# Performance work log

Hardware: AMD Instinct MI355X
Metric: run time of the kernel (lower is better)

Reference implementation:

```python
import jax, jax.numpy as jnp
import numpy as np
from math import erf, pi, sqrt, exp

D = 2048
TARGET_BITS = 2.5
N_HIGH = 1024  # round(D * frac)
N_LOW = D - N_HIGH
HIGH_MSE_BITS = 2  # ceil(2.5) - 1
LOW_MSE_BITS = 1   # floor(2.5) - 1


def _phi(x):
    return np.exp(-0.5 * x * x) / np.sqrt(2.0 * np.pi)


def _Phi(x):
    return 0.5 * (1.0 + np.vectorize(erf)(x / np.sqrt(2.0)))


def lloyd_max_centroids(bits: int) -> np.ndarray:
    """Lloyd-Max optimal scalar quantizer centroids for N(0,1), 2**bits levels."""
    L = 2 ** bits
    c = np.linspace(-2.0, 2.0, L)
    for _ in range(200):
        b = 0.5 * (c[:-1] + c[1:])                      # decision boundaries
        edges = np.concatenate([[-1e9], b, [1e9]])
        lo, hi = edges[:-1], edges[1:]
        mass = _Phi(hi) - _Phi(lo)
        c = (_phi(lo) - _phi(hi)) / np.maximum(mass, 1e-12)  # conditional mean
    return c.astype(np.float32)


def generate_rotation_matrix(d: int, seed: int) -> np.ndarray:
    rng = np.random.default_rng(seed)
    A = rng.standard_normal((d, d)).astype(np.float64)
    Q, R = np.linalg.qr(A)
    Q = Q * np.sign(np.diag(R))[None, :]
    return Q.astype(np.float32)


def setup_inputs() -> dict:
    key = jax.random.key(0)
    kq, kk = jax.random.split(key)
    queries = jax.random.normal(kq, (1024, D), dtype=jnp.float32)
    keys = jax.random.normal(kk, (4096, D), dtype=jnp.float32)
    Pi = jnp.asarray(generate_rotation_matrix(D, seed=42 + 2000))
    high_centroids = jnp.asarray(lloyd_max_centroids(HIGH_MSE_BITS))  # (4,)
    low_centroids = jnp.asarray(lloyd_max_centroids(LOW_MSE_BITS))    # (2,)
    rng = np.random.default_rng(42)
    S_high = jnp.asarray(rng.standard_normal((N_HIGH, N_HIGH)).astype(np.float32))
    rng2 = np.random.default_rng(42 + 1000)
    S_low = jnp.asarray(rng2.standard_normal((N_LOW, N_LOW)).astype(np.float32))
    return {"queries": queries, "keys": keys, "Pi": Pi,
            "high_centroids": high_centroids, "low_centroids": low_centroids,
            "S_high": S_high, "S_low": S_low}


def _quantize_group(y, centroids, S):
    # nearest-centroid scalar quantization per channel
    idx = jnp.argmin(jnp.abs(y[..., None] - centroids), axis=-1)  # (bk, n_ch)
    y_mse = centroids[idx]
    residual = y - y_mse
    residual_norm = jnp.linalg.norm(residual, axis=-1)            # (bk,)
    signs = jnp.sign(residual @ S.T)                              # (bk, m)
    return y_mse, signs, residual_norm


def _ip_group(q_ch, y_mse, signs, residual_norm, S):
    m = S.shape[0]
    term1 = q_ch @ y_mse.T                                        # (bq, bk)
    # QJL estimator: <q, r> ~ sqrt(pi/2)/m * ||r|| * <S q, sign(S r)>
    term2 = (jnp.sqrt(jnp.float32(pi / 2)) / m) * ((q_ch @ S.T) @ signs.T) * residual_norm[None, :]
    return term1 + term2


def reference(queries, keys, Pi, high_centroids, low_centroids, S_high, S_low):
    # ---- quantize keys ----
    vec_norm = jnp.linalg.norm(keys, axis=-1)                     # (bk,)
    k_n = keys / (vec_norm[:, None] + 1e-8)
    y = k_n @ Pi.T
    yh, yl = y[:, :N_HIGH], y[:, N_HIGH:]
    kmse_h, sg_h, rn_h = _quantize_group(yh, high_centroids, S_high)
    kmse_l, sg_l, rn_l = _quantize_group(yl, low_centroids, S_low)
    # ---- inner product estimate ----
    q_rot = queries @ Pi.T
    qh, ql = q_rot[:, :N_HIGH], q_rot[:, N_HIGH:]
    ip = _ip_group(qh, kmse_h, sg_h, rn_h, S_high) + _ip_group(ql, kmse_l, sg_l, rn_l, S_low)
    return ip * vec_norm[None, :]                                 # (bq, bk)
```

## Files before the change

### kernel.cpp

```cpp
#include <hip/hip_runtime.h>
#include <math.h>

#ifndef M_PI
#define M_PI 3.14159265358979323846
#endif

typedef __attribute__((ext_vector_type(8))) __bf16 bf16x8;
typedef __attribute__((ext_vector_type(4))) float f32x4;
typedef __attribute__((ext_vector_type(8))) unsigned short ushort8;

__device__ __forceinline__ unsigned short f2bf(float x) {
    unsigned int u = __float_as_uint(x);
    unsigned int r = (u + 0x7FFFu + ((u >> 16) & 1u)) >> 16;
    return (unsigned short)r;
}

__global__ __launch_bounds__(256)
void norm_np_k(const float* __restrict__ keys,
               float* __restrict__ den,
               float* __restrict__ vnorm)
{
#pragma clang fp contract(off)
    const int tid = threadIdx.x;
    const int row_l = tid >> 4;
    const int blk = tid & 15;
    const int row = blockIdx.x * 16 + row_l;
    const float* a = keys + (size_t)row * 2048 + blk * 128;

    float r0 = a[0]*a[0], r1 = a[1]*a[1], r2 = a[2]*a[2], r3 = a[3]*a[3];
    float r4 = a[4]*a[4], r5 = a[5]*a[5], r6 = a[6]*a[6], r7 = a[7]*a[7];
    for (int i = 8; i < 128; i += 8) {
        r0 += a[i+0]*a[i+0]; r1 += a[i+1]*a[i+1];
        r2 += a[i+2]*a[i+2]; r3 += a[i+3]*a[i+3];
        r4 += a[i+4]*a[i+4]; r5 += a[i+5]*a[i+5];
        r6 += a[i+6]*a[i+6]; r7 += a[i+7]*a[i+7];
    }
    float bsum = ((r0 + r1) + (r2 + r3)) + ((r4 + r5) + (r6 + r7));

    __shared__ float bs[16][16];
    bs[row_l][blk] = bsum;
    __syncthreads();
    if (blk == 0) {
        const float* b = bs[row_l];
        float q0 = ((b[0] + b[1]) + (b[2] + b[3])) + ((b[4] + b[5]) + (b[6] + b[7]));
        float q1 = ((b[8] + b[9]) + (b[10] + b[11])) + ((b[12] + b[13]) + (b[14] + b[15]));
        float s = q0 + q1;
        float n = (float)sqrt((double)s);
        den[row] = n + 1e-8f;
        vnorm[row] = n;
    }
}

__global__ __launch_bounds__(256)
void f2bf_k(const float* __restrict__ in, unsigned short* __restrict__ out)
{
    const int i = (blockIdx.x * 256 + threadIdx.x) * 8;
    float4 v0 = *(const float4*)(in + i);
    float4 v1 = *(const float4*)(in + i + 4);
    ushort8 o;
    o[0] = f2bf(v0.x); o[1] = f2bf(v0.y); o[2] = f2bf(v0.z); o[3] = f2bf(v0.w);
    o[4] = f2bf(v1.x); o[5] = f2bf(v1.y); o[6] = f2bf(v1.z); o[7] = f2bf(v1.w);
    *(ushort8*)(out + i) = o;
}

template <int EPI, int DIVA>
__global__ __launch_bounds__(256)
void gemm_dec_k(const float* __restrict__ A, int lda,
                const float* __restrict__ B, int ldb,
                float* __restrict__ Cf, unsigned short* __restrict__ Cb,
                int ldc, int K,
                const float* __restrict__ dena,
                const float* __restrict__ rv)
{
#pragma clang fp contract(off)
    __shared__ float As[16][132];
    __shared__ float Bs[16][132];

    const int tid = threadIdx.x;
    const int tr = tid >> 4;
    const int tc = tid & 15;
    const int row0 = blockIdx.y * 128;
    const int col0 = blockIdx.x * 128;
    const int sr = tid >> 1;
    const int sk = (tid & 1) * 8;

    const float dv = DIVA ? dena[row0 + sr] : 1.0f;
    const float* ga = A + (size_t)(row0 + sr) * lda + sk;
    const float* gb = B + (size_t)(col0 + sr) * ldb + sk;

    float acc[8][8] = {};

    for (int k0 = 0; k0 < K; k0 += 16) {
        float av[8], bv[8];
        *(float4*)(av)     = *(const float4*)(ga + k0);
        *(float4*)(av + 4) = *(const float4*)(ga + k0 + 4);
        *(float4*)(bv)     = *(const float4*)(gb + k0);
        *(float4*)(bv + 4) = *(const float4*)(gb + k0 + 4);
        if (DIVA) {
            #pragma unroll
            for (int u = 0; u < 8; ++u) av[u] = av[u] / dv;
        }
        __syncthreads();
        #pragma unroll
        for (int u = 0; u < 8; ++u) {
            As[sk + u][sr] = av[u];
            Bs[sk + u][sr] = bv[u];
        }
        __syncthreads();
        #pragma unroll
        for (int kk = 0; kk < 16; ++kk) {
            float a[8], b[8];
            *(float4*)(a)     = *(const float4*)&As[kk][tr * 8];
            *(float4*)(a + 4) = *(const float4*)&As[kk][tr * 8 + 4];
            *(float4*)(b)     = *(const float4*)&Bs[kk][tc * 8];
            *(float4*)(b + 4) = *(const float4*)&Bs[kk][tc * 8 + 4];
            #pragma unroll
            for (int i = 0; i < 8; ++i)
                #pragma unroll
                for (int j = 0; j < 8; ++j)
                    acc[i][j] = fmaf(a[i], b[j], acc[i][j]);
        }
    }

    if (EPI == 0) {
        #pragma unroll
        for (int i = 0; i < 8; ++i) {
            const int r = row0 + tr * 8 + i;
            #pragma unroll
            for (int j = 0; j < 8; ++j)
                Cf[(size_t)r * ldc + col0 + tc * 8 + j] = acc[i][j];
        }
    } else {
        #pragma unroll
        for (int i = 0; i < 8; ++i) {
            const int r = row0 + tr * 8 + i;
            const float s = rv[r];
            #pragma unroll
            for (int j = 0; j < 8; ++j) {
                const float t = acc[i][j];
                const float v = (t > 0.0f) ? s : ((t < 0.0f) ? -s : 0.0f);
                Cb[(size_t)r * ldc + col0 + tc * 8 + j] = f2bf(v);
            }
        }
    }
}

__global__ __launch_bounds__(256)
void quant_k(float* __restrict__ Y,
             unsigned short* __restrict__ Bmse,
             const float* __restrict__ ch,
             const float* __restrict__ cl,
             float* __restrict__ sc_h,
             float* __restrict__ sc_l,
             double coefd)
{
#pragma clang fp contract(off)
    const int row = blockIdx.x;
    const int tid = threadIdx.x;
    const int c0 = tid * 8;
    const float h0 = ch[0], h1 = ch[1], h2 = ch[2], h3 = ch[3];
    const float l0 = cl[0], l1 = cl[1];

    float y[8], res[8];
    ushort8 cb;
    *(float4*)(y)     = *(const float4*)(Y + (size_t)row * 2048 + c0);
    *(float4*)(y + 4) = *(const float4*)(Y + (size_t)row * 2048 + c0 + 4);

    const bool high = (tid < 128);
    float ss = 0.0f;
    #pragma unroll
    for (int j = 0; j < 8; ++j) {
        const float v = y[j];
        float cbest;
        if (high) {
            cbest = h0;
            float bd = fabsf(v - h0), dd;
            dd = fabsf(v - h1); if (dd < bd) { bd = dd; cbest = h1; }
            dd = fabsf(v - h2); if (dd < bd) { bd = dd; cbest = h2; }
            dd = fabsf(v - h3); if (dd < bd) { bd = dd; cbest = h3; }
        } else {
            cbest = (fabsf(v - l1) < fabsf(v - l0)) ? l1 : l0;
        }
        res[j] = v - cbest;
        cb[j] = f2bf(cbest);
        ss += res[j] * res[j];
    }
    *(float4*)(Y + (size_t)row * 2048 + c0)     = *(float4*)(res);
    *(float4*)(Y + (size_t)row * 2048 + c0 + 4) = *(float4*)(res + 4);
    *(ushort8*)(Bmse + (size_t)row * 4096 + c0) = cb;

    __shared__ float sm[256];
    sm[tid] = ss;
    __syncthreads();
    for (int o = 64; o > 0; o >>= 1) {
        if ((tid & 127) < o) sm[tid] += sm[tid + o];
        __syncthreads();
    }
    if (tid == 0)   sc_h[row] = (float)(coefd * sqrt((double)sm[0]));
    if (tid == 128) sc_l[row] = (float)(coefd * sqrt((double)sm[128]));
}

template <int EPI>
__global__ __launch_bounds__(256)
void gemm_mfma_k(const unsigned short* __restrict__ A, int lda,
                 const unsigned short* __restrict__ B, int ldb,
                 float* __restrict__ Cf, unsigned short* __restrict__ Cb,
                 int ldc, int K, const float* __restrict__ colscale)
{
    __shared__ unsigned short As[128][40];
    __shared__ unsigned short Bs[128][40];

    const int tid = threadIdx.x;
    const int lane = tid & 63;
    const int wid = tid >> 6;
    const int wm = wid >> 1;
    const int wn = wid & 1;
    const int row0 = blockIdx.y * 128;
    const int col0 = blockIdx.x * 128;
    const int sr = tid >> 1;
    const int sk = (tid & 1) * 16;
    const int frow = lane & 15;
    const int fk = (lane >> 4) * 8;

    const unsigned short* ga = A + (size_t)(row0 + sr) * lda + sk;
    const unsigned short* gb = B + (size_t)(col0 + sr) * ldb + sk;

    f32x4 acc[4][4] = {};

    for (int k0 = 0; k0 < K; k0 += 32) {
        ushort8 a0 = *(const ushort8*)(ga + k0);
        ushort8 a1 = *(const ushort8*)(ga + k0 + 8);
        ushort8 b0 = *(const ushort8*)(gb + k0);
        ushort8 b1 = *(const ushort8*)(gb + k0 + 8);
        __syncthreads();
        *(ushort8*)&As[sr][sk]     = a0;
        *(ushort8*)&As[sr][sk + 8] = a1;
        *(ushort8*)&Bs[sr][sk]     = b0;
        *(ushort8*)&Bs[sr][sk + 8] = b1;
        __syncthreads();

        bf16x8 af[4], bfr[4];
        #pragma unroll
        for (int mi = 0; mi < 4; ++mi)
            af[mi] = *(const bf16x8*)&As[wm * 64 + mi * 16 + frow][fk];
        #pragma unroll
        for (int ni = 0; ni < 4; ++ni)
            bfr[ni] = *(const bf16x8*)&Bs[wn * 64 + ni * 16 + frow][fk];
        #pragma unroll
        for (int mi = 0; mi < 4; ++mi)
            #pragma unroll
            for (int ni = 0; ni < 4; ++ni)
                acc[mi][ni] = __builtin_amdgcn_mfma_f32_16x16x32_bf16(
                    af[mi], bfr[ni], acc[mi][ni], 0, 0, 0);
    }

    const int drow = (lane >> 4) * 4;
    const int dcol = lane & 15;
    #pragma unroll
    for (int mi = 0; mi < 4; ++mi) {
        #pragma unroll
        for (int ni = 0; ni < 4; ++ni) {
            const int c = col0 + wn * 64 + ni * 16 + dcol;
            const float cs = (EPI == 1) ? colscale[c] : 0.0f;
            #pragma unroll
            for (int rg = 0; rg < 4; ++rg) {
                const int r = row0 + wm * 64 + mi * 16 + drow + rg;
                const float v = acc[mi][ni][rg];
                if (EPI == 1) Cf[(size_t)r * ldc + c] = v * cs;
                else          Cb[(size_t)r * ldc + c] = f2bf(v);
            }
        }
    }
}

extern "C" void kernel_launch(void* const* d_in, const int* in_sizes, int n_in,
                              void* d_out, int out_size, void* d_ws, size_t ws_size,
                              hipStream_t stream)
{
    const float* queries = (const float*)d_in[0];
    const float* keys    = (const float*)d_in[1];
    const float* Pi      = (const float*)d_in[2];
    const float* ch      = (const float*)d_in[3];
    const float* cl      = (const float*)d_in[4];
    const float* S_high  = (const float*)d_in[5];
    const float* S_low   = (const float*)d_in[6];
    float* out = (float*)d_out;

    char* ws = (char*)d_ws;
    float*          Y     = (float*)(ws);
    unsigned short* Bbig  = (unsigned short*)(ws + ((size_t)32 << 20));
    unsigned short* Abig  = (unsigned short*)(ws + ((size_t)64 << 20));
    unsigned short* Qb    = (unsigned short*)(ws + ((size_t)72 << 20));
    unsigned short* Pib   = (unsigned short*)(ws + ((size_t)76 << 20));
    unsigned short* Sbh   = (unsigned short*)(ws + ((size_t)84 << 20));
    unsigned short* Sbl   = (unsigned short*)(ws + ((size_t)86 << 20));
    float*          den   = (float*)(ws + ((size_t)88 << 20));
    float*          vnorm = (float*)(ws + ((size_t)88 << 20) + 16384);
    float*          sc_h  = (float*)(ws + ((size_t)88 << 20) + 32768);
    float*          sc_l  = (float*)(ws + ((size_t)88 << 20) + 49152);

    const double coefd = sqrt(M_PI / 2.0) / 1024.0;

    norm_np_k<<<256, 256, 0, stream>>>(keys, den, vnorm);

    f2bf_k<<<1024, 256, 0, stream>>>(queries, Qb);
    f2bf_k<<<2048, 256, 0, stream>>>(Pi, Pib);
    f2bf_k<<<512, 256, 0, stream>>>(S_high, Sbh);
    f2bf_k<<<512, 256, 0, stream>>>(S_low, Sbl);

    gemm_dec_k<0, 1><<<dim3(16, 32), 256, 0, stream>>>(
        keys, 2048, Pi, 2048, Y, nullptr, 2048, 2048, den, nullptr);

    quant_k<<<4096, 256, 0, stream>>>(Y, Bbig, ch, cl, sc_h, sc_l, coefd);

    gemm_dec_k<1, 0><<<dim3(8, 32), 256, 0, stream>>>(
        Y, 2048, S_high, 1024, nullptr, Bbig + 2048, 4096, 1024, nullptr, sc_h);
    gemm_dec_k<1, 0><<<dim3(8, 32), 256, 0, stream>>>(
        Y + 1024, 2048, S_low, 1024, nullptr, Bbig + 3072, 4096, 1024, nullptr, sc_l);

    gemm_mfma_k<2><<<dim3(16, 8), 256, 0, stream>>>(
        Qb, 2048, Pib, 2048, nullptr, Abig, 4096, 2048, nullptr);
    gemm_mfma_k<2><<<dim3(8, 8), 256, 0, stream>>>(
        Abig, 4096, Sbh, 1024, nullptr, Abig + 2048, 4096, 1024, nullptr);
    gemm_mfma_k<2><<<dim3(8, 8), 256, 0, stream>>>(
        Abig + 1024, 4096, Sbl, 1024, nullptr, Abig + 3072, 4096, 1024, nullptr);

    gemm_mfma_k<1><<<dim3(32, 8), 256, 0, stream>>>(
        Abig, 4096, Bbig, 4096, out, nullptr, 4096, 4096, vnorm);
}
```

Before: 940.9 us.

## Prefetch and double-buffer fp32 GEMM fragments, batch per-group GEMMs via grid z

The fp32 exact GEMM now prefetches the next global K-slab into registers while it computes the current one. It also double-buffers the LDS fragment reads and remaps each thread's 8x8 tile into two 4-wide strips spaced 64 apart, so LDS reads avoid bank conflicts and stores can be vectorized. The key normalization divide moves into a separate elementwise kernel that writes a normalized copy of the keys. The high and low QJL sign GEMMs, and the two S-projection MFMA GEMMs, each merge into a single launch using blockIdx.z. This removes launches and fills more CUs, at the cost of an extra 32MB read/write pass for the normalized keys.

New measurement: 829.2 us. -11.9%, faster.

```diff
diff --git a/kernel.cpp b/kernel.cpp
--- a/kernel.cpp
+++ b/kernel.cpp
@@ -8,6 +8,7 @@
 typedef __attribute__((ext_vector_type(8))) __bf16 bf16x8;
 typedef __attribute__((ext_vector_type(4))) float f32x4;
 typedef __attribute__((ext_vector_type(8))) unsigned short ushort8;
+typedef __attribute__((ext_vector_type(4))) unsigned short ushort4v;
 
 __device__ __forceinline__ unsigned short f2bf(float x) {
     unsigned int u = __float_as_uint(x);
@@ -52,6 +53,23 @@
 }
 
 __global__ __launch_bounds__(256)
+void kn_k(const float* __restrict__ keys,
+          const float* __restrict__ den,
+          float* __restrict__ kn)
+{
+#pragma clang fp contract(off)
+    const int idx = (blockIdx.x * 256 + threadIdx.x) * 8;
+    const int row = idx >> 11;
+    const float d = den[row];
+    float4 v0 = *(const float4*)(keys + idx);
+    float4 v1 = *(const float4*)(keys + idx + 4);
+    v0.x /= d; v0.y /= d; v0.z /= d; v0.w /= d;
+    v1.x /= d; v1.y /= d; v1.z /= d; v1.w /= d;
+    *(float4*)(kn + idx) = v0;
+    *(float4*)(kn + idx + 4) = v1;
+}
+
+__global__ __launch_bounds__(256)
 void f2bf_k(const float* __restrict__ in, unsigned short* __restrict__ out)
 {
     const int i = (blockIdx.x * 256 + threadIdx.x) * 8;
@@ -63,86 +81,116 @@
     *(ushort8*)(out + i) = o;
 }
 
-template <int EPI, int DIVA>
-__global__ __launch_bounds__(256)
-void gemm_dec_k(const float* __restrict__ A, int lda,
-                const float* __restrict__ B, int ldb,
+template <int EPI>
+__global__ __launch_bounds__(256)
+void gemm_dec_k(const float* __restrict__ A, int lda, int a_zoff,
+                const float* __restrict__ B0, const float* __restrict__ B1,
+                int ldb,
                 float* __restrict__ Cf, unsigned short* __restrict__ Cb,
-                int ldc, int K,
-                const float* __restrict__ dena,
-                const float* __restrict__ rv)
+                int c_zoff, int ldc, int K,
+                const float* __restrict__ rv0, const float* __restrict__ rv1)
 {
 #pragma clang fp contract(off)
     __shared__ float As[16][132];
     __shared__ float Bs[16][132];
 
+    const int z = blockIdx.z;
+    const float* Ap = A + (size_t)z * a_zoff;
+    const float* Bp = z ? B1 : B0;
+    const float* rvp = z ? rv1 : rv0;
+    unsigned short* Cbp = (EPI == 1) ? (Cb + (size_t)z * c_zoff) : nullptr;
+
     const int tid = threadIdx.x;
-    const int tr = tid >> 4;
-    const int tc = tid & 15;
+    const int tr4 = (tid >> 4) * 4;
+    const int tc4 = (tid & 15) * 4;
     const int row0 = blockIdx.y * 128;
     const int col0 = blockIdx.x * 128;
     const int sr = tid >> 1;
     const int sk = (tid & 1) * 8;
 
-    const float dv = DIVA ? dena[row0 + sr] : 1.0f;
-    const float* ga = A + (size_t)(row0 + sr) * lda + sk;
-    const float* gb = B + (size_t)(col0 + sr) * ldb + sk;
-
-    float acc[8][8] = {};
+    const float* ga = Ap + (size_t)(row0 + sr) * lda + sk;
+    const float* gb = Bp + (size_t)(col0 + sr) * ldb + sk;
+
+    float acc[2][2][4][4] = {};
+    float sa[8], sb[8];
+
+#define LOADSTAGE(off) do { \
+    *(float4*)(sa)     = *(const float4*)(ga + (off)); \
+    *(float4*)(sa + 4) = *(const float4*)(ga + (off) + 4); \
+    *(float4*)(sb)     = *(const float4*)(gb + (off)); \
+    *(float4*)(sb + 4) = *(const float4*)(gb + (off) + 4); \
+} while (0)
+
+#define RDFRAG(fa, fb, kk) do { \
+    *(float4*)(fa)     = *(const float4*)&As[kk][tr4]; \
+    *(float4*)(fa + 4) = *(const float4*)&As[kk][tr4 + 64]; \
+    *(float4*)(fb)     = *(const float4*)&Bs[kk][tc4]; \
+    *(float4*)(fb + 4) = *(const float4*)&Bs[kk][tc4 + 64]; \
+} while (0)
+
+#define FMAS(fa, fb) do { \
+    _Pragma("unroll") \
+    for (int mb = 0; mb < 2; ++mb) \
+        _Pragma("unroll") \
+        for (int i = 0; i < 4; ++i) \
+            _Pragma("unroll") \
+            for (int nb = 0; nb < 2; ++nb) \
+                _Pragma("unroll") \
+                for (int j = 0; j < 4; ++j) \
+                    acc[mb][nb][i][j] = fmaf((fa)[mb*4+i], (fb)[nb*4+j], acc[mb][nb][i][j]); \
+} while (0)
+
+    LOADSTAGE(0);
 
     for (int k0 = 0; k0 < K; k0 += 16) {
-        float av[8], bv[8];
-        *(float4*)(av)     = *(const float4*)(ga + k0);
-        *(float4*)(av + 4) = *(const float4*)(ga + k0 + 4);
-        *(float4*)(bv)     = *(const float4*)(gb + k0);
-        *(float4*)(bv + 4) = *(const float4*)(gb + k0 + 4);
-        if (DIVA) {
-            #pragma unroll
-            for (int u = 0; u < 8; ++u) av[u] = av[u] / dv;
-        }
         __syncthreads();
         #pragma unroll
         for (int u = 0; u < 8; ++u) {
-            As[sk + u][sr] = av[u];
-            Bs[sk + u][sr] = bv[u];
-        }
-        __syncthreads();
-        #pragma unroll
-        for (int kk = 0; kk < 16; ++kk) {
-            float a[8], b[8];
-            *(float4*)(a)     = *(const float4*)&As[kk][tr * 8];
-            *(float4*)(a + 4) = *(const float4*)&As[kk][tr * 8 + 4];
-            *(float4*)(b)     = *(const float4*)&Bs[kk][tc * 8];
-            *(float4*)(b + 4) = *(const float4*)&Bs[kk][tc * 8 + 4];
-            #pragma unroll
-            for (int i = 0; i < 8; ++i)
+            As[sk + u][sr] = sa[u];
+            Bs[sk + u][sr] = sb[u];
+        }
+        __syncthreads();
+        if (k0 + 16 < K) LOADSTAGE(k0 + 16);
+
+        float fa0[8], fb0[8], fa1[8], fb1[8];
+        RDFRAG(fa0, fb0, 0);
+        #pragma unroll
+        for (int kk = 0; kk < 16; kk += 2) {
+            RDFRAG(fa1, fb1, kk + 1);
+            FMAS(fa0, fb0);
+            if (kk + 2 < 16) RDFRAG(fa0, fb0, kk + 2);
+            FMAS(fa1, fb1);
+        }
+    }
+
+    #pragma unroll
+    for (int mb = 0; mb < 2; ++mb) {
+        #pragma unroll
+        for (int i = 0; i < 4; ++i) {
+            const int r = row0 + mb * 64 + tr4 + i;
+            if (EPI == 0) {
                 #pragma unroll
-                for (int j = 0; j < 8; ++j)
-                    acc[i][j] = fmaf(a[i], b[j], acc[i][j]);
-        }
-    }
-
-    if (EPI == 0) {
-        #pragma unroll
-        for (int i = 0; i < 8; ++i) {
-            const int r = row0 + tr * 8 + i;
-            #pragma unroll
-            for (int j = 0; j < 8; ++j)
-                Cf[(size_t)r * ldc + col0 + tc * 8 + j] = acc[i][j];
-        }
-    } else {
-        #pragma unroll
-        for (int i = 0; i < 8; ++i) {
-            const int r = row0 + tr * 8 + i;
-            const float s = rv[r];
-            #pragma unroll
-            for (int j = 0; j < 8; ++j) {
-                const float t = acc[i][j];
-                const float v = (t > 0.0f) ? s : ((t < 0.0f) ? -s : 0.0f);
-                Cb[(size_t)r * ldc + col0 + tc * 8 + j] = f2bf(v);
+                for (int nb = 0; nb < 2; ++nb)
+                    *(float4*)&Cf[(size_t)r * ldc + col0 + nb * 64 + tc4] =
+                        *(const float4*)&acc[mb][nb][i][0];
+            } else {
+                const float s = rvp[r];
+                #pragma unroll
+                for (int nb = 0; nb < 2; ++nb) {
+                    ushort4v o;
+                    #pragma unroll
+                    for (int j = 0; j < 4; ++j) {
+                        const float t = acc[mb][nb][i][j];
+                        o[j] = f2bf((t > 0.0f) ? s : ((t < 0.0f) ? -s : 0.0f));
+                    }
+                    *(ushort4v*)&Cbp[(size_t)r * ldc + col0 + nb * 64 + tc4] = o;
+                }
             }
         }
     }
+#undef LOADSTAGE
+#undef RDFRAG
+#undef FMAS
 }
 
 __global__ __launch_bounds__(256)
@@ -202,13 +250,20 @@
 
 template <int EPI>
 __global__ __launch_bounds__(256)
-void gemm_mfma_k(const unsigned short* __restrict__ A, int lda,
-                 const unsigned short* __restrict__ B, int ldb,
+void gemm_mfma_k(const unsigned short* __restrict__ A, int lda, int a_zoff,
+                 const unsigned short* __restrict__ B0,
+                 const unsigned short* __restrict__ B1, int ldb,
                  float* __restrict__ Cf, unsigned short* __restrict__ Cb,
-                 int ldc, int K, const float* __restrict__ colscale)
+                 int c_zoff, int ldc, int K,
+                 const float* __restrict__ colscale)
 {
     __shared__ unsigned short As[128][40];
     __shared__ unsigned short Bs[128][40];
+
+    const int z = blockIdx.z;
+    const unsigned short* Ap = A + (size_t)z * a_zoff;
+    const unsigned short* Bp = z ? B1 : B0;
+    unsigned short* Cbp = (EPI == 2) ? (Cb + (size_t)z * c_zoff) : nullptr;
 
     const int tid = threadIdx.x;
     const int lane = tid & 63;
@@ -222,8 +277,8 @@
     const int frow = lane & 15;
     const int fk = (lane >> 4) * 8;
 
-    const unsigned short* ga = A + (size_t)(row0 + sr) * lda + sk;
-    const unsigned short* gb = B + (size_t)(col0 + sr) * ldb + sk;
+    const unsigned short* ga = Ap + (size_t)(row0 + sr) * lda + sk;
+    const unsigned short* gb = Bp + (size_t)(col0 + sr) * ldb + sk;
 
     f32x4 acc[4][4] = {};
 
@@ -267,7 +322,7 @@
                 const int r = row0 + wm * 64 + mi * 16 + drow + rg;
                 const float v = acc[mi][ni][rg];
                 if (EPI == 1) Cf[(size_t)r * ldc + c] = v * cs;
-                else          Cb[(size_t)r * ldc + c] = f2bf(v);
+                else          Cbp[(size_t)r * ldc + c] = f2bf(v);
             }
         }
     }
@@ -287,44 +342,44 @@
     float* out = (float*)d_out;
 
     char* ws = (char*)d_ws;
-    float*          Y     = (float*)(ws);
-    unsigned short* Bbig  = (unsigned short*)(ws + ((size_t)32 << 20));
-    unsigned short* Abig  = (unsigned short*)(ws + ((size_t)64 << 20));
-    unsigned short* Qb    = (unsigned short*)(ws + ((size_t)72 << 20));
-    unsigned short* Pib   = (unsigned short*)(ws + ((size_t)76 << 20));
-    unsigned short* Sbh   = (unsigned short*)(ws + ((size_t)84 << 20));
-    unsigned short* Sbl   = (unsigned short*)(ws + ((size_t)86 << 20));
-    float*          den   = (float*)(ws + ((size_t)88 << 20));
-    float*          vnorm = (float*)(ws + ((size_t)88 << 20) + 16384);
-    float*          sc_h  = (float*)(ws + ((size_t)88 << 20) + 32768);
-    float*          sc_l  = (float*)(ws + ((size_t)88 << 20) + 49152);
+    float*          kn    = (float*)(ws);
+    float*          Y     = (float*)(ws + ((size_t)32 << 20));
+    unsigned short* Bbig  = (unsigned short*)(ws + ((size_t)64 << 20));
+    unsigned short* Abig  = (unsigned short*)(ws + ((size_t)96 << 20));
+    unsigned short* Qb    = (unsigned short*)(ws + ((size_t)104 << 20));
+    unsigned short* Pib   = (unsigned short*)(ws + ((size_t)108 << 20));
+    unsigned short* Sbh   = (unsigned short*)(ws + ((size_t)116 << 20));
+    unsigned short* Sbl   = (unsigned short*)(ws + ((size_t)118 << 20));
+    float*          den   = (float*)(ws + ((size_t)120 << 20));
+    float*          vnorm = (float*)(ws + ((size_t)120 << 20) + 16384);
+    float*          sc_h  = (float*)(ws + ((size_t)120 << 20) + 32768);
+    float*          sc_l  = (float*)(ws + ((size_t)120 << 20) + 49152);
 
     const double coefd = sqrt(M_PI / 2.0) / 1024.0;
 
     norm_np_k<<<256, 256, 0, stream>>>(keys, den, vnorm);
+
+    kn_k<<<4096, 256, 0, stream>>>(keys, den, kn);
 
     f2bf_k<<<1024, 256, 0, stream>>>(queries, Qb);
     f2bf_k<<<2048, 256, 0, stream>>>(Pi, Pib);
     f2bf_k<<<512, 256, 0, stream>>>(S_high, Sbh);
     f2bf_k<<<512, 256, 0, stream>>>(S_low, Sbl);
 
-    gemm_dec_k<0, 1><<<dim3(16, 32), 256, 0, stream>>>(
-        keys, 2048, Pi, 2048, Y, nullptr, 2048, 2048, den, nullptr);
+    gemm_dec_k<0><<<dim3(16, 32, 1), 256, 0, stream>>>(
+        kn, 2048, 0, Pi, Pi, 2048, Y, nullptr, 0, 2048, 2048, nullptr, nullptr);
 
     quant_k<<<4096, 256, 0, stream>>>(Y, Bbig, ch, cl, sc_h, sc_l, coefd);
 
-    gemm_dec_k<1, 0><<<dim3(8, 32), 256, 0, stream>>>(
-        Y, 2048, S_high, 1024, nullptr, Bbig + 2048, 4096, 1024, nullptr, sc_h);
-    gemm_dec_k<1, 0><<<dim3(8, 32), 256, 0, stream>>>(
-        Y + 1024, 2048, S_low, 1024, nullptr, Bbig + 3072, 4096, 1024, nullptr, sc_l);
-
-    gemm_mfma_k<2><<<dim3(16, 8), 256, 0, stream>>>(
-        Qb, 2048, Pib, 2048, nullptr, Abig, 4096, 2048, nullptr);
-    gemm_mfma_k<2><<<dim3(8, 8), 256, 0, stream>>>(
-        Abig, 4096, Sbh, 1024, nullptr, Abig + 2048, 4096, 1024, nullptr);
-    gemm_mfma_k<2><<<dim3(8, 8), 256, 0, stream>>>(
-        Abig + 1024, 4096, Sbl, 1024, nullptr, Abig + 3072, 4096, 1024, nullptr);
-
-    gemm_mfma_k<1><<<dim3(32, 8), 256, 0, stream>>>(
-        Abig, 4096, Bbig, 4096, out, nullptr, 4096, 4096, vnorm);
-}
+    gemm_dec_k<1><<<dim3(8, 32, 2), 256, 0, stream>>>(
+        Y, 2048, 1024, S_high, S_low, 1024,
+        nullptr, Bbig + 2048, 1024, 4096, 1024, sc_h, sc_l);
+
+    gemm_mfma_k<2><<<dim3(16, 8, 1), 256, 0, stream>>>(
+        Qb, 2048, 0, Pib, Pib, 2048, nullptr, Abig, 0, 4096, 2048, nullptr);
+    gemm_mfma_k<2><<<dim3(8, 8, 2), 256, 0, stream>>>(
+        Abig, 4096, 1024, Sbh, Sbl, 1024, nullptr, Abig + 2048, 1024, 4096, 1024, nullptr);
+
+    gemm_mfma_k<1><<<dim3(32, 8, 1), 256, 0, stream>>>(
+        Abig, 4096, 0, Bbig, Bbig, 4096, out, nullptr, 0, 4096, 4096, vnorm);
+}
```
